# Kernel optimization log

Measured on AMD Instinct MI355X. Metric: run time of the kernel, lower is better.

The kernel has to match this reference:

```python
import jax, jax.numpy as jnp
import numpy as np

N = 100000      # nodes
E = 1600000     # directed edges (avg degree 16)
F_IN = 256      # dataset.num_node_features
HID = 64        # hidden
C = 40          # dataset.num_classes


def setup_inputs() -> dict:
    key = jax.random.key(0)
    k0, k1, k2, k3 = jax.random.split(key, 4)
    x = jax.random.normal(k0, (N, F_IN), dtype=jnp.float32)
    edge_index = jax.random.randint(k1, (2, E), 0, N, dtype=jnp.int32)
    # Glorot-style init like GCNConv.reset_parameters
    W1 = jax.random.normal(k2, (F_IN, HID), dtype=jnp.float32) * (1.0 / np.sqrt(F_IN))
    b1 = jnp.zeros((HID,), dtype=jnp.float32)
    W2 = jax.random.normal(k3, (HID, C), dtype=jnp.float32) * (1.0 / np.sqrt(HID))
    b2 = jnp.zeros((C,), dtype=jnp.float32)
    return {"x": x, "edge_index": edge_index, "W1": W1, "b1": b1, "W2": W2, "b2": b2}


def gcn_conv(x, row, col, norm, W, b):
    # PyG GCNConv: out[col] += norm * (x @ W)[row]; then + bias
    n = x.shape[0]
    h = x @ W                                   # [N, out]
    msg = h[row] * norm[:, None]                # [E+N, out] gather + scale
    out = jax.ops.segment_sum(msg, col, num_segments=n)  # scatter-add
    return out + b


def _norm_coeffs(edge_index, n, dtype):
    # add self-loops, then symmetric normalization D^{-1/2} A D^{-1/2}
    loop = jnp.arange(n, dtype=edge_index.dtype)
    row = jnp.concatenate([edge_index[0], loop])
    col = jnp.concatenate([edge_index[1], loop])
    deg = jax.ops.segment_sum(jnp.ones_like(col, dtype=dtype), col, num_segments=n)
    dis = jnp.where(deg > 0, jax.lax.rsqrt(jnp.maximum(deg, 1.0)), 0.0)
    return row, col, dis[row] * dis[col]


def reference(x, edge_index, W1, b1, W2, b2):
    n = x.shape[0]
    row, col, norm = _norm_coeffs(edge_index, n, x.dtype)
    h = jax.nn.relu(gcn_conv(x, row, col, norm, W1, b1))
    # F.dropout(p=0.5, training=False) is identity in eval mode
    out = gcn_conv(h, row, col, norm, W2, b2)
    return jax.nn.log_softmax(out, axis=1)
```

## Files before the change

### kernel.cpp

```cpp
#include <hip/hip_runtime.h>
#include <math.h>

#define N_NODES 100000
#define N_EDGES 1600000
#define F_INDIM 256
#define HID 64
#define NCLS 40
#define NBKT 196
#define NBLKA 196
#define EPB 8192
#define CAPB 96
#define REGSZ 12544
#define ECAP 10240
#define NGEMM1 391
#define KP 264
#define AP 72

typedef __attribute__((ext_vector_type(8))) short short8;
typedef __attribute__((ext_vector_type(4))) float floatx4;

__device__ __forceinline__ unsigned short f2bf(float f) {
  unsigned u = __float_as_uint(f);
  unsigned r = (u + 0x7FFFu + ((u >> 16) & 1u)) >> 16;
  return (unsigned short)r;
}
__device__ __forceinline__ void add8(float* a, uint4 u) {
  a[0] += __uint_as_float(u.x << 16);
  a[1] += __uint_as_float(u.x & 0xFFFF0000u);
  a[2] += __uint_as_float(u.y << 16);
  a[3] += __uint_as_float(u.y & 0xFFFF0000u);
  a[4] += __uint_as_float(u.z << 16);
  a[5] += __uint_as_float(u.z & 0xFFFF0000u);
  a[6] += __uint_as_float(u.w << 16);
  a[7] += __uint_as_float(u.w & 0xFFFF0000u);
}
__device__ __forceinline__ void fma8(float* a, float d, uint4 u) {
  a[0] = fmaf(d, __uint_as_float(u.x << 16), a[0]);
  a[1] = fmaf(d, __uint_as_float(u.x & 0xFFFF0000u), a[1]);
  a[2] = fmaf(d, __uint_as_float(u.y << 16), a[2]);
  a[3] = fmaf(d, __uint_as_float(u.y & 0xFFFF0000u), a[3]);
  a[4] = fmaf(d, __uint_as_float(u.z << 16), a[4]);
  a[5] = fmaf(d, __uint_as_float(u.z & 0xFFFF0000u), a[5]);
  a[6] = fmaf(d, __uint_as_float(u.w << 16), a[6]);
  a[7] = fmaf(d, __uint_as_float(u.w & 0xFFFF0000u), a[7]);
}


__global__ __launch_bounds__(1024) void k_pre(const int* __restrict__ row,
                                              const int* __restrict__ col,
                                              const float* __restrict__ x,
                                              const float* __restrict__ W1,
                                              unsigned int* __restrict__ bktdata,
                                              int* __restrict__ cnt,
                                              unsigned short* __restrict__ h1b) {
  __shared__ union {
    int cur[NBKT];
    unsigned short wt[HID * KP];
  } sm;
  const int t = threadIdx.x;

  if (blockIdx.x < NBLKA) {
    const int blk = blockIdx.x;
    const int e0 = blk * EPB;
    const int n = min(EPB, N_EDGES - e0);
    if (t < NBKT) sm.cur[t] = 0;
    __syncthreads();
    for (int i = t * 4; i < n; i += 4096) {
      int4 c4 = *(const int4*)&col[e0 + i];
      int4 r4 = *(const int4*)&row[e0 + i];
#pragma unroll
      for (int k = 0; k < 4; ++k) {
        int c = (k == 0) ? c4.x : (k == 1) ? c4.y : (k == 2) ? c4.z : c4.w;
        int r = (k == 0) ? r4.x : (k == 1) ? r4.y : (k == 2) ? r4.z : r4.w;
        int b = c >> 9;
        int p = atomicAdd(&sm.cur[b], 1);
        if (p < CAPB)
          bktdata[((size_t)b * NBLKA + blk) * CAPB + p] =
              ((unsigned)(c & 511) << 17) | (unsigned)r;
      }
    }
    __syncthreads();
    if (t < NBKT) cnt[t * NBLKA + blk] = min(sm.cur[t], CAPB);
  } else {
    const int lane = t & 63;
    const int w = t >> 6;
    const int quad = lane >> 4;
    const int l15 = lane & 15;
    const int rowBase = (blockIdx.x - NBLKA) * 256;
#pragma unroll
    for (int i = 0; i < 4; ++i) {
      int f = t + 1024 * i;
      int k = f >> 4;
      int n0 = (f & 15) * 4;
      float4 v = *(const float4*)&W1[(size_t)k * HID + n0];
      sm.wt[(n0 + 0) * KP + k] = f2bf(v.x);
      sm.wt[(n0 + 1) * KP + k] = f2bf(v.y);
      sm.wt[(n0 + 2) * KP + k] = f2bf(v.z);
      sm.wt[(n0 + 3) * KP + k] = f2bf(v.w);
    }
    __syncthreads();

    const int ar = rowBase + w * 16 + l15;
    const float* xrow =
        x + (size_t)((ar < N_NODES) ? ar : N_NODES - 1) * F_INDIM + quad * 8;

    floatx4 acc[4];
#pragma unroll
    for (int c = 0; c < 4; ++c) acc[c] = (floatx4){0.f, 0.f, 0.f, 0.f};

#pragma unroll
    for (int kc = 0; kc < F_INDIM; kc += 32) {
      const float4 va = *(const float4*)(xrow + kc);
      const float4 vb = *(const float4*)(xrow + kc + 4);
      short8 a;
      a[0] = (short)f2bf(va.x); a[1] = (short)f2bf(va.y);
      a[2] = (short)f2bf(va.z); a[3] = (short)f2bf(va.w);
      a[4] = (short)f2bf(vb.x); a[5] = (short)f2bf(vb.y);
      a[6] = (short)f2bf(vb.z); a[7] = (short)f2bf(vb.w);
#pragma unroll
      for (int c = 0; c < 4; ++c) {
        const short8 bfr = *(const short8*)&sm.wt[(c * 16 + l15) * KP + kc + quad * 8];
        acc[c] = __builtin_amdgcn_mfma_f32_16x16x32_bf16(a, bfr, acc[c], 0, 0, 0);
      }
    }

#pragma unroll
    for (int reg = 0; reg < 4; ++reg) {
      int gr = rowBase + w * 16 + quad * 4 + reg;
      if (gr <= N_NODES) {
        bool real = gr < N_NODES;
#pragma unroll
        for (int c = 0; c < 4; ++c)
          h1b[(size_t)gr * HID + c * 16 + l15] =
              real ? f2bf(acc[c][reg]) : (unsigned short)0;
      }
    }
  }
}


__global__ __launch_bounds__(1024) void k_build2(const int* __restrict__ cnt,
                                                 const unsigned int* __restrict__ bktdata,
                                                 float* __restrict__ dis,
                                                 int* __restrict__ start,
                                                 int* __restrict__ endi,
                                                 int* __restrict__ esrc) {
  __shared__ int scnt[NBLKA];
  __shared__ int sscan[NBLKA];
  __shared__ unsigned int ecache[ECAP];
  __shared__ int h[512];
  __shared__ int curs[512];
  __shared__ int sbase[512];
  const int b = blockIdx.x, t = threadIdx.x;

  if (t < 512) { h[t] = 0; curs[t] = 0; }
  if (t < NBLKA) { int c = cnt[b * NBLKA + t]; scnt[t] = c; sscan[t] = c; }
  __syncthreads();
#pragma unroll
  for (int off = 1; off < NBLKA; off <<= 1) {
    int u = (t < NBLKA && t >= off) ? sscan[t - off] : 0;
    __syncthreads();
    if (t < NBLKA) sscan[t] += u;
    __syncthreads();
  }
  const int total = min(sscan[NBLKA - 1], ECAP);

  for (int j = t; j < total; j += 1024) {
    int lo = 0, hi = NBLKA - 1;
    while (lo < hi) {
      int mid = (lo + hi) >> 1;
      if (sscan[mid] <= j) lo = mid + 1; else hi = mid;
    }
    int segoff = j - (sscan[lo] - scnt[lo]);
    ecache[j] = bktdata[((size_t)b * NBLKA + lo) * CAPB + segoff];
  }
  __syncthreads();

  for (int i = t; i < total; i += 1024) atomicAdd(&h[ecache[i] >> 17], 1);
  __syncthreads();

  int c0 = 0, p0 = 0;
  if (t < 512) {
    const int n0 = b * 512 + t;
    c0 = h[t];
    p0 = (c0 + 7) & ~7;
    if (n0 < N_NODES) dis[n0] = rsqrtf((float)(c0 + 1));
    else if (n0 == N_NODES) dis[n0] = 0.f;
    h[t] = p0;
  }
  __syncthreads();
#pragma unroll
  for (int off = 1; off < 512; off <<= 1) {
    int u = (t < 512 && t >= off) ? h[t - off] : 0;
    __syncthreads();
    if (t < 512) h[t] += u;
    __syncthreads();
  }
  if (t < 512) {
    const int n0 = b * 512 + t;
    const int sb0 = b * REGSZ + h[t] - p0;
    sbase[t] = sb0;
    if (n0 < N_NODES) { start[n0] = sb0; endi[n0] = sb0 + c0; }
    for (int k = c0; k < p0; ++k) esrc[sb0 + k] = N_NODES;
  }
  __syncthreads();

  for (int i = t; i < total; i += 1024) {
    unsigned u = ecache[i];
    int ld = u >> 17;
    int src = u & 0x1FFFF;
    int pos = sbase[ld] + atomicAdd(&curs[ld], 1);
    esrc[pos] = src;
  }
}


__global__ __launch_bounds__(512) void k_agg1g2(const int* __restrict__ esrc,
                                                const int* __restrict__ start,
                                                const int* __restrict__ endi,
                                                const float* __restrict__ dis,
                                                const unsigned short* __restrict__ h1b,
                                                const float* __restrict__ b1,
                                                const float* __restrict__ W2,
                                                unsigned short* __restrict__ gb) {
  __shared__ unsigned short as[64 * AP];
  __shared__ unsigned short w2t[48 * AP];
  const int t = threadIdx.x;
  const int nodeBase = blockIdx.x * 64;
  const int node = nodeBase + (t >> 3);
  const int q = t & 7;

  for (int i = t; i < 48 * 64; i += 512) {
    int nn = i >> 6;
    int k = i & 63;
    w2t[nn * AP + k] = (nn < NCLS) ? f2bf(W2[(size_t)k * NCLS + nn]) : (unsigned short)0;
  }

  uint4 o = (uint4){0u, 0u, 0u, 0u};
  if (node < N_NODES) {
    const uint4* hp4 = (const uint4*)h1b;
    const int s = start[node];
    const int e8 = (endi[node] + 7) & ~7;
    float acc[8];
#pragma unroll
    for (int j = 0; j < 8; ++j) acc[j] = 0.f;
    for (int i = s; i < e8; i += 8) {
      int4 sa = *(const int4*)&esrc[i];
      int4 sb = *(const int4*)&esrc[i + 4];
      float d0 = dis[sa.x], d1 = dis[sa.y], d2 = dis[sa.z], d3 = dis[sa.w];
      float d4 = dis[sb.x], d5 = dis[sb.y], d6 = dis[sb.z], d7 = dis[sb.w];
      uint4 u0 = hp4[(size_t)sa.x * 8 + q];
      uint4 u1 = hp4[(size_t)sa.y * 8 + q];
      uint4 u2 = hp4[(size_t)sa.z * 8 + q];
      uint4 u3 = hp4[(size_t)sa.w * 8 + q];
      uint4 u4 = hp4[(size_t)sb.x * 8 + q];
      uint4 u5 = hp4[(size_t)sb.y * 8 + q];
      uint4 u6 = hp4[(size_t)sb.z * 8 + q];
      uint4 u7 = hp4[(size_t)sb.w * 8 + q];
      fma8(acc, d0, u0); fma8(acc, d1, u1); fma8(acc, d2, u2); fma8(acc, d3, u3);
      fma8(acc, d4, u4); fma8(acc, d5, u5); fma8(acc, d6, u6); fma8(acc, d7, u7);
    }
    const float dn = dis[node];
    uint4 us = hp4[(size_t)node * 8 + q];
    fma8(acc, dn, us);
    float4 ba = *(const float4*)&b1[q * 8];
    float4 bb = *(const float4*)&b1[q * 8 + 4];
    float v0 = fmaxf(dn * acc[0] + ba.x, 0.f);
    float v1 = fmaxf(dn * acc[1] + ba.y, 0.f);
    float v2 = fmaxf(dn * acc[2] + ba.z, 0.f);
    float v3 = fmaxf(dn * acc[3] + ba.w, 0.f);
    float v4 = fmaxf(dn * acc[4] + bb.x, 0.f);
    float v5 = fmaxf(dn * acc[5] + bb.y, 0.f);
    float v6 = fmaxf(dn * acc[6] + bb.z, 0.f);
    float v7 = fmaxf(dn * acc[7] + bb.w, 0.f);
    o.x = (unsigned)f2bf(v0) | ((unsigned)f2bf(v1) << 16);
    o.y = (unsigned)f2bf(v2) | ((unsigned)f2bf(v3) << 16);
    o.z = (unsigned)f2bf(v4) | ((unsigned)f2bf(v5) << 16);
    o.w = (unsigned)f2bf(v6) | ((unsigned)f2bf(v7) << 16);
  }
  *(uint4*)&as[(t >> 3) * AP + q * 8] = o;
  __syncthreads();

  const int lane = t & 63;
  const int w = t >> 6;
  if (w < 4) {
    const int quad = lane >> 4;
    const int l15 = lane & 15;
    floatx4 acc2[3];
#pragma unroll
    for (int c = 0; c < 3; ++c) acc2[c] = (floatx4){0.f, 0.f, 0.f, 0.f};
#pragma unroll
    for (int kh = 0; kh < 2; ++kh) {
      const short8 a = *(const short8*)&as[(w * 16 + l15) * AP + kh * 32 + quad * 8];
#pragma unroll
      for (int c = 0; c < 3; ++c) {
        const short8 bfr = *(const short8*)&w2t[(c * 16 + l15) * AP + kh * 32 + quad * 8];
        acc2[c] = __builtin_amdgcn_mfma_f32_16x16x32_bf16(a, bfr, acc2[c], 0, 0, 0);
      }
    }
#pragma unroll
    for (int reg = 0; reg < 4; ++reg) {
      int gr = nodeBase + w * 16 + quad * 4 + reg;
      if (gr <= N_NODES) {
        float dd = dis[gr];
#pragma unroll
        for (int c = 0; c < 3; ++c)
          gb[(size_t)gr * 64 + c * 16 + l15] = f2bf(dd * acc2[c][reg]);
        gb[(size_t)gr * 64 + 48 + l15] = 0;
      }
    }
  }
}


__global__ __launch_bounds__(256) void k_agg2ls(const int* __restrict__ esrc,
                                                const int* __restrict__ start,
                                                const int* __restrict__ endi,
                                                const float* __restrict__ dis,
                                                const unsigned short* __restrict__ gb,
                                                const float* __restrict__ b2,
                                                float* __restrict__ out) {
  int gid = blockIdx.x * 256 + threadIdx.x;
  int node = gid >> 3;
  int q = gid & 7;
  if (node >= N_NODES) return;
  const uint4* gp4 = (const uint4*)gb;
  const int s = start[node];
  const int e8 = (endi[node] + 7) & ~7;
  float acc[8];
#pragma unroll
  for (int j = 0; j < 8; ++j) acc[j] = 0.f;
  for (int i = s; i < e8; i += 8) {
    int4 sa = *(const int4*)&esrc[i];
    int4 sb = *(const int4*)&esrc[i + 4];
    uint4 u0 = gp4[(size_t)sa.x * 8 + q];
    uint4 u1 = gp4[(size_t)sa.y * 8 + q];
    uint4 u2 = gp4[(size_t)sa.z * 8 + q];
    uint4 u3 = gp4[(size_t)sa.w * 8 + q];
    uint4 u4 = gp4[(size_t)sb.x * 8 + q];
    uint4 u5 = gp4[(size_t)sb.y * 8 + q];
    uint4 u6 = gp4[(size_t)sb.z * 8 + q];
    uint4 u7 = gp4[(size_t)sb.w * 8 + q];
    add8(acc, u0); add8(acc, u1); add8(acc, u2); add8(acc, u3);
    add8(acc, u4); add8(acc, u5); add8(acc, u6); add8(acc, u7);
  }
  uint4 us = gp4[(size_t)node * 8 + q];
  add8(acc, us);
  const bool wr = q < 5;
  float v0 = 0.f, v1 = 0.f, v2 = 0.f, v3 = 0.f, v4 = 0.f, v5 = 0.f, v6 = 0.f, v7 = 0.f;
  float m = -INFINITY;
  if (wr) {
    float d = dis[node];
    float4 ba = *(const float4*)&b2[q * 8];
    float4 bb = *(const float4*)&b2[q * 8 + 4];
    v0 = d * acc[0] + ba.x;
    v1 = d * acc[1] + ba.y;
    v2 = d * acc[2] + ba.z;
    v3 = d * acc[3] + ba.w;
    v4 = d * acc[4] + bb.x;
    v5 = d * acc[5] + bb.y;
    v6 = d * acc[6] + bb.z;
    v7 = d * acc[7] + bb.w;
    m = fmaxf(fmaxf(fmaxf(v0, v1), fmaxf(v2, v3)),
              fmaxf(fmaxf(v4, v5), fmaxf(v6, v7)));
  }
#pragma unroll
  for (int off = 1; off < 8; off <<= 1) m = fmaxf(m, __shfl_xor(m, off));
  float el = 0.f;
  if (wr) {
    el = __expf(v0 - m) + __expf(v1 - m) + __expf(v2 - m) + __expf(v3 - m) +
         __expf(v4 - m) + __expf(v5 - m) + __expf(v6 - m) + __expf(v7 - m);
  }
#pragma unroll
  for (int off = 1; off < 8; off <<= 1) el += __shfl_xor(el, off);
  float ls = logf(el);
  if (wr) {
    float4 o1 = make_float4(v0 - m - ls, v1 - m - ls, v2 - m - ls, v3 - m - ls);
    float4 o2 = make_float4(v4 - m - ls, v5 - m - ls, v6 - m - ls, v7 - m - ls);
    *(float4*)&out[(size_t)node * NCLS + q * 8] = o1;
    *(float4*)&out[(size_t)node * NCLS + q * 8 + 4] = o2;
  }
}


extern "C" void kernel_launch(void* const* d_in, const int* in_sizes, int n_in,
                              void* d_out, int out_size, void* d_ws, size_t ws_size,
                              hipStream_t stream) {
  const float* x  = (const float*)d_in[0];
  const int*   ei = (const int*)d_in[1];
  const float* W1 = (const float*)d_in[2];
  const float* b1 = (const float*)d_in[3];
  const float* W2 = (const float*)d_in[4];
  const float* b2 = (const float*)d_in[5];
  float* out = (float*)d_out;

  const int* row = ei;
  const int* col = ei + N_EDGES;

  int*            esrc    = (int*)d_ws;
  unsigned int*   bktdata = (unsigned int*)(esrc + (size_t)NBKT * REGSZ);
  int*            cnt     = (int*)(bktdata + (size_t)NBKT * NBLKA * CAPB);
  unsigned short* h1b     = (unsigned short*)(cnt + NBKT * NBLKA);
  unsigned short* gb      = h1b + (size_t)(N_NODES + 1) * HID;
  float*          dis     = (float*)(gb + (size_t)(N_NODES + 1) * HID);
  int*            start   = (int*)(dis + N_NODES + 1);
  int*            endi    = start + N_NODES + 1;

  k_pre<<<NBLKA + NGEMM1, 1024, 0, stream>>>(row, col, x, W1, bktdata, cnt, h1b);
  k_build2<<<NBKT, 1024, 0, stream>>>(cnt, bktdata, dis, start, endi, esrc);
  k_agg1g2<<<(N_NODES + 63) / 64, 512, 0, stream>>>(esrc, start, endi, dis, h1b, b1, W2, gb);
  k_agg2ls<<<(N_NODES * 8 + 255) / 256, 256, 0, stream>>>(esrc, start, endi, dis, gb, b2, out);
}
```

Baseline: 316.2 us.

## Prescale layer-1 features by dis and split aggregation from second GEMM

```diff
diff --git a/kernel.cpp b/kernel.cpp
--- a/kernel.cpp
+++ b/kernel.cpp
@@ -34,16 +34,6 @@
   a[6] += __uint_as_float(u.w << 16);
   a[7] += __uint_as_float(u.w & 0xFFFF0000u);
 }
-__device__ __forceinline__ void fma8(float* a, float d, uint4 u) {
-  a[0] = fmaf(d, __uint_as_float(u.x << 16), a[0]);
-  a[1] = fmaf(d, __uint_as_float(u.x & 0xFFFF0000u), a[1]);
-  a[2] = fmaf(d, __uint_as_float(u.y << 16), a[2]);
-  a[3] = fmaf(d, __uint_as_float(u.y & 0xFFFF0000u), a[3]);
-  a[4] = fmaf(d, __uint_as_float(u.z << 16), a[4]);
-  a[5] = fmaf(d, __uint_as_float(u.z & 0xFFFF0000u), a[5]);
-  a[6] = fmaf(d, __uint_as_float(u.w << 16), a[6]);
-  a[7] = fmaf(d, __uint_as_float(u.w & 0xFFFF0000u), a[7]);
-}
 
 
 __global__ __launch_bounds__(1024) void k_pre(const int* __restrict__ row,
@@ -144,13 +134,15 @@
                                                  float* __restrict__ dis,
                                                  int* __restrict__ start,
                                                  int* __restrict__ endi,
-                                                 int* __restrict__ esrc) {
+                                                 int* __restrict__ esrc,
+                                                 unsigned short* __restrict__ h1b) {
   __shared__ int scnt[NBLKA];
   __shared__ int sscan[NBLKA];
   __shared__ unsigned int ecache[ECAP];
   __shared__ int h[512];
   __shared__ int curs[512];
   __shared__ int sbase[512];
+  __shared__ float sdis[512];
   const int b = blockIdx.x, t = threadIdx.x;
 
   if (t < 512) { h[t] = 0; curs[t] = 0; }
@@ -184,8 +176,9 @@
     const int n0 = b * 512 + t;
     c0 = h[t];
     p0 = (c0 + 7) & ~7;
-    if (n0 < N_NODES) dis[n0] = rsqrtf((float)(c0 + 1));
-    else if (n0 == N_NODES) dis[n0] = 0.f;
+    float dv = rsqrtf((float)(c0 + 1));
+    sdis[t] = (n0 < N_NODES) ? dv : 0.f;
+    if (n0 < N_NODES) dis[n0] = dv;
     h[t] = p0;
   }
   __syncthreads();
@@ -212,102 +205,137 @@
     int pos = sbase[ld] + atomicAdd(&curs[ld], 1);
     esrc[pos] = src;
   }
-}
-
-
-__global__ __launch_bounds__(512) void k_agg1g2(const int* __restrict__ esrc,
-                                                const int* __restrict__ start,
-                                                const int* __restrict__ endi,
-                                                const float* __restrict__ dis,
-                                                const unsigned short* __restrict__ h1b,
-                                                const float* __restrict__ b1,
-                                                const float* __restrict__ W2,
-                                                unsigned short* __restrict__ gb) {
+
+  uint4* h4 = (uint4*)h1b;
+  for (int i = t; i < 512 * 8; i += 1024) {
+    int r = i >> 3, qq = i & 7;
+    int n0 = b * 512 + r;
+    if (n0 < N_NODES) {
+      float d = sdis[r];
+      uint4 u = h4[(size_t)n0 * 8 + qq];
+      float f0 = __uint_as_float(u.x << 16) * d;
+      float f1 = __uint_as_float(u.x & 0xFFFF0000u) * d;
+      float f2 = __uint_as_float(u.y << 16) * d;
+      float f3 = __uint_as_float(u.y & 0xFFFF0000u) * d;
+      float f4 = __uint_as_float(u.z << 16) * d;
+      float f5 = __uint_as_float(u.z & 0xFFFF0000u) * d;
+      float f6 = __uint_as_float(u.w << 16) * d;
+      float f7 = __uint_as_float(u.w & 0xFFFF0000u) * d;
+      u.x = (unsigned)f2bf(f0) | ((unsigned)f2bf(f1) << 16);
+      u.y = (unsigned)f2bf(f2) | ((unsigned)f2bf(f3) << 16);
+      u.z = (unsigned)f2bf(f4) | ((unsigned)f2bf(f5) << 16);
+      u.w = (unsigned)f2bf(f6) | ((unsigned)f2bf(f7) << 16);
+      h4[(size_t)n0 * 8 + qq] = u;
+    }
+  }
+}
+
+
+__global__ __launch_bounds__(256) void k_agg1(const int* __restrict__ esrc,
+                                              const int* __restrict__ start,
+                                              const int* __restrict__ endi,
+                                              const float* __restrict__ dis,
+                                              const unsigned short* __restrict__ h1b,
+                                              const float* __restrict__ b1,
+                                              unsigned short* __restrict__ ab) {
+  int gid = blockIdx.x * 256 + threadIdx.x;
+  int node = gid >> 3;
+  int q = gid & 7;
+  if (node >= N_NODES) return;
+  const uint4* hp4 = (const uint4*)h1b;
+  const int s = start[node];
+  const int e8 = (endi[node] + 7) & ~7;
+  float acc[8];
+#pragma unroll
+  for (int j = 0; j < 8; ++j) acc[j] = 0.f;
+  for (int i = s; i < e8; i += 8) {
+    int4 sa = *(const int4*)&esrc[i];
+    int4 sb = *(const int4*)&esrc[i + 4];
+    uint4 u0 = hp4[(size_t)sa.x * 8 + q];
+    uint4 u1 = hp4[(size_t)sa.y * 8 + q];
+    uint4 u2 = hp4[(size_t)sa.z * 8 + q];
+    uint4 u3 = hp4[(size_t)sa.w * 8 + q];
+    uint4 u4 = hp4[(size_t)sb.x * 8 + q];
+    uint4 u5 = hp4[(size_t)sb.y * 8 + q];
+    uint4 u6 = hp4[(size_t)sb.z * 8 + q];
+    uint4 u7 = hp4[(size_t)sb.w * 8 + q];
+    add8(acc, u0); add8(acc, u1); add8(acc, u2); add8(acc, u3);
+    add8(acc, u4); add8(acc, u5); add8(acc, u6); add8(acc, u7);
+  }
+  uint4 us = hp4[(size_t)node * 8 + q];
+  add8(acc, us);
+  float d = dis[node];
+  float4 ba = *(const float4*)&b1[q * 8];
+  float4 bb = *(const float4*)&b1[q * 8 + 4];
+  float v0 = fmaxf(d * acc[0] + ba.x, 0.f);
+  float v1 = fmaxf(d * acc[1] + ba.y, 0.f);
+  float v2 = fmaxf(d * acc[2] + ba.z, 0.f);
+  float v3 = fmaxf(d * acc[3] + ba.w, 0.f);
+  float v4 = fmaxf(d * acc[4] + bb.x, 0.f);
+  float v5 = fmaxf(d * acc[5] + bb.y, 0.f);
+  float v6 = fmaxf(d * acc[6] + bb.z, 0.f);
+  float v7 = fmaxf(d * acc[7] + bb.w, 0.f);
+  uint4 o;
+  o.x = (unsigned)f2bf(v0) | ((unsigned)f2bf(v1) << 16);
+  o.y = (unsigned)f2bf(v2) | ((unsigned)f2bf(v3) << 16);
+  o.z = (unsigned)f2bf(v4) | ((unsigned)f2bf(v5) << 16);
+  o.w = (unsigned)f2bf(v6) | ((unsigned)f2bf(v7) << 16);
+  ((uint4*)ab)[(size_t)node * 8 + q] = o;
+}
+
+
+__global__ __launch_bounds__(256) void k_gemm2(const unsigned short* __restrict__ ab,
+                                               const float* __restrict__ W2,
+                                               const float* __restrict__ dis,
+                                               unsigned short* __restrict__ gb) {
   __shared__ unsigned short as[64 * AP];
   __shared__ unsigned short w2t[48 * AP];
-  const int t = threadIdx.x;
-  const int nodeBase = blockIdx.x * 64;
-  const int node = nodeBase + (t >> 3);
-  const int q = t & 7;
-
-  for (int i = t; i < 48 * 64; i += 512) {
-    int nn = i >> 6;
+  const int tid = threadIdx.x;
+  const int lane = tid & 63;
+  const int w = tid >> 6;
+  const int quad = lane >> 4;
+  const int l15 = lane & 15;
+  const int rowBase = blockIdx.x * 64;
+
+  for (int i = tid; i < 48 * 64; i += 256) {
+    int n = i >> 6;
     int k = i & 63;
-    w2t[nn * AP + k] = (nn < NCLS) ? f2bf(W2[(size_t)k * NCLS + nn]) : (unsigned short)0;
-  }
-
-  uint4 o = (uint4){0u, 0u, 0u, 0u};
-  if (node < N_NODES) {
-    const uint4* hp4 = (const uint4*)h1b;
-    const int s = start[node];
-    const int e8 = (endi[node] + 7) & ~7;
-    float acc[8];
-#pragma unroll
-    for (int j = 0; j < 8; ++j) acc[j] = 0.f;
-    for (int i = s; i < e8; i += 8) {
-      int4 sa = *(const int4*)&esrc[i];
-      int4 sb = *(const int4*)&esrc[i + 4];
-      float d0 = dis[sa.x], d1 = dis[sa.y], d2 = dis[sa.z], d3 = dis[sa.w];
-      float d4 = dis[sb.x], d5 = dis[sb.y], d6 = dis[sb.z], d7 = dis[sb.w];
-      uint4 u0 = hp4[(size_t)sa.x * 8 + q];
-      uint4 u1 = hp4[(size_t)sa.y * 8 + q];
-      uint4 u2 = hp4[(size_t)sa.z * 8 + q];
-      uint4 u3 = hp4[(size_t)sa.w * 8 + q];
-      uint4 u4 = hp4[(size_t)sb.x * 8 + q];
-      uint4 u5 = hp4[(size_t)sb.y * 8 + q];
-      uint4 u6 = hp4[(size_t)sb.z * 8 + q];
-      uint4 u7 = hp4[(size_t)sb.w * 8 + q];
-      fma8(acc, d0, u0); fma8(acc, d1, u1); fma8(acc, d2, u2); fma8(acc, d3, u3);
-      fma8(acc, d4, u4); fma8(acc, d5, u5); fma8(acc, d6, u6); fma8(acc, d7, u7);
-    }
-    const float dn = dis[node];
-    uint4 us = hp4[(size_t)node * 8 + q];
-    fma8(acc, dn, us);
-    float4 ba = *(const float4*)&b1[q * 8];
-    float4 bb = *(const float4*)&b1[q * 8 + 4];
-    float v0 = fmaxf(dn * acc[0] + ba.x, 0.f);
-    float v1 = fmaxf(dn * acc[1] + ba.y, 0.f);
-    float v2 = fmaxf(dn * acc[2] + ba.z, 0.f);
-    float v3 = fmaxf(dn * acc[3] + ba.w, 0.f);
-    float v4 = fmaxf(dn * acc[4] + bb.x, 0.f);
-    float v5 = fmaxf(dn * acc[5] + bb.y, 0.f);
-    float v6 = fmaxf(dn * acc[6] + bb.z, 0.f);
-    float v7 = fmaxf(dn * acc[7] + bb.w, 0.f);
-    o.x = (unsigned)f2bf(v0) | ((unsigned)f2bf(v1) << 16);
-    o.y = (unsigned)f2bf(v2) | ((unsigned)f2bf(v3) << 16);
-    o.z = (unsigned)f2bf(v4) | ((unsigned)f2bf(v5) << 16);
-    o.w = (unsigned)f2bf(v6) | ((unsigned)f2bf(v7) << 16);
-  }
-  *(uint4*)&as[(t >> 3) * AP + q * 8] = o;
-  __syncthreads();
-
-  const int lane = t & 63;
-  const int w = t >> 6;
-  if (w < 4) {
-    const int quad = lane >> 4;
-    const int l15 = lane & 15;
-    floatx4 acc2[3];
-#pragma unroll
-    for (int c = 0; c < 3; ++c) acc2[c] = (floatx4){0.f, 0.f, 0.f, 0.f};
-#pragma unroll
-    for (int kh = 0; kh < 2; ++kh) {
-      const short8 a = *(const short8*)&as[(w * 16 + l15) * AP + kh * 32 + quad * 8];
-#pragma unroll
-      for (int c = 0; c < 3; ++c) {
-        const short8 bfr = *(const short8*)&w2t[(c * 16 + l15) * AP + kh * 32 + quad * 8];
-        acc2[c] = __builtin_amdgcn_mfma_f32_16x16x32_bf16(a, bfr, acc2[c], 0, 0, 0);
-      }
-    }
-#pragma unroll
-    for (int reg = 0; reg < 4; ++reg) {
-      int gr = nodeBase + w * 16 + quad * 4 + reg;
-      if (gr <= N_NODES) {
-        float dd = dis[gr];
-#pragma unroll
-        for (int c = 0; c < 3; ++c)
-          gb[(size_t)gr * 64 + c * 16 + l15] = f2bf(dd * acc2[c][reg]);
-        gb[(size_t)gr * 64 + 48 + l15] = 0;
-      }
+    w2t[n * AP + k] = (n < NCLS) ? f2bf(W2[(size_t)k * NCLS + n]) : (unsigned short)0;
+  }
+#pragma unroll
+  for (int i = 0; i < 2; ++i) {
+    int f = tid + 256 * i;
+    int r = f >> 3;
+    int q = f & 7;
+    int gr = rowBase + r;
+    short8 v = (short8){0, 0, 0, 0, 0, 0, 0, 0};
+    if (gr < N_NODES) v = *(const short8*)&ab[(size_t)gr * HID + q * 8];
+    *(short8*)&as[r * AP + q * 8] = v;
+  }
+  __syncthreads();
+
+  floatx4 acc[3];
+#pragma unroll
+  for (int c = 0; c < 3; ++c) acc[c] = (floatx4){0.f, 0.f, 0.f, 0.f};
+
+#pragma unroll
+  for (int kh = 0; kh < 2; ++kh) {
+    const short8 a = *(const short8*)&as[(w * 16 + l15) * AP + kh * 32 + quad * 8];
+#pragma unroll
+    for (int c = 0; c < 3; ++c) {
+      const short8 bfr = *(const short8*)&w2t[(c * 16 + l15) * AP + kh * 32 + quad * 8];
+      acc[c] = __builtin_amdgcn_mfma_f32_16x16x32_bf16(a, bfr, acc[c], 0, 0, 0);
+    }
+  }
+
+#pragma unroll
+  for (int reg = 0; reg < 4; ++reg) {
+    int gr = rowBase + w * 16 + quad * 4 + reg;
+    if (gr < N_NODES) {
+      float d = dis[gr];
+#pragma unroll
+      for (int c = 0; c < 3; ++c)
+        gb[(size_t)gr * 64 + c * 16 + l15] = f2bf(d * acc[c][reg]);
     }
   }
 }
@@ -324,29 +352,31 @@
   int node = gid >> 3;
   int q = gid & 7;
   if (node >= N_NODES) return;
-  const uint4* gp4 = (const uint4*)gb;
-  const int s = start[node];
-  const int e8 = (endi[node] + 7) & ~7;
+  const bool wr = q < 5;
   float acc[8];
 #pragma unroll
   for (int j = 0; j < 8; ++j) acc[j] = 0.f;
-  for (int i = s; i < e8; i += 8) {
-    int4 sa = *(const int4*)&esrc[i];
-    int4 sb = *(const int4*)&esrc[i + 4];
-    uint4 u0 = gp4[(size_t)sa.x * 8 + q];
-    uint4 u1 = gp4[(size_t)sa.y * 8 + q];
-    uint4 u2 = gp4[(size_t)sa.z * 8 + q];
-    uint4 u3 = gp4[(size_t)sa.w * 8 + q];
-    uint4 u4 = gp4[(size_t)sb.x * 8 + q];
-    uint4 u5 = gp4[(size_t)sb.y * 8 + q];
-    uint4 u6 = gp4[(size_t)sb.z * 8 + q];
-    uint4 u7 = gp4[(size_t)sb.w * 8 + q];
-    add8(acc, u0); add8(acc, u1); add8(acc, u2); add8(acc, u3);
-    add8(acc, u4); add8(acc, u5); add8(acc, u6); add8(acc, u7);
-  }
-  uint4 us = gp4[(size_t)node * 8 + q];
-  add8(acc, us);
-  const bool wr = q < 5;
+  if (wr) {
+    const uint4* gp4 = (const uint4*)gb;
+    const int s = start[node];
+    const int e8 = (endi[node] + 7) & ~7;
+    for (int i = s; i < e8; i += 8) {
+      int4 sa = *(const int4*)&esrc[i];
+      int4 sb = *(const int4*)&esrc[i + 4];
+      uint4 u0 = gp4[(size_t)sa.x * 8 + q];
+      uint4 u1 = gp4[(size_t)sa.y * 8 + q];
+      uint4 u2 = gp4[(size_t)sa.z * 8 + q];
+      uint4 u3 = gp4[(size_t)sa.w * 8 + q];
+      uint4 u4 = gp4[(size_t)sb.x * 8 + q];
+      uint4 u5 = gp4[(size_t)sb.y * 8 + q];
+      uint4 u6 = gp4[(size_t)sb.z * 8 + q];
+      uint4 u7 = gp4[(size_t)sb.w * 8 + q];
+      add8(acc, u0); add8(acc, u1); add8(acc, u2); add8(acc, u3);
+      add8(acc, u4); add8(acc, u5); add8(acc, u6); add8(acc, u7);
+    }
+    uint4 us = gp4[(size_t)node * 8 + q];
+    add8(acc, us);
+  }
   float v0 = 0.f, v1 = 0.f, v2 = 0.f, v3 = 0.f, v4 = 0.f, v5 = 0.f, v6 = 0.f, v7 = 0.f;
   float m = -INFINITY;
   if (wr) {
@@ -401,13 +431,15 @@
   unsigned int*   bktdata = (unsigned int*)(esrc + (size_t)NBKT * REGSZ);
   int*            cnt     = (int*)(bktdata + (size_t)NBKT * NBLKA * CAPB);
   unsigned short* h1b     = (unsigned short*)(cnt + NBKT * NBLKA);
-  unsigned short* gb      = h1b + (size_t)(N_NODES + 1) * HID;
-  float*          dis     = (float*)(gb + (size_t)(N_NODES + 1) * HID);
-  int*            start   = (int*)(dis + N_NODES + 1);
-  int*            endi    = start + N_NODES + 1;
+  unsigned short* ab      = h1b + (size_t)(N_NODES + 1) * HID;
+  float*          dis     = (float*)(ab + (size_t)N_NODES * HID);
+  int*            start   = (int*)(dis + N_NODES);
+  int*            endi    = start + N_NODES;
+  unsigned short* gb      = h1b;
 
   k_pre<<<NBLKA + NGEMM1, 1024, 0, stream>>>(row, col, x, W1, bktdata, cnt, h1b);
-  k_build2<<<NBKT, 1024, 0, stream>>>(cnt, bktdata, dis, start, endi, esrc);
-  k_agg1g2<<<(N_NODES + 63) / 64, 512, 0, stream>>>(esrc, start, endi, dis, h1b, b1, W2, gb);
+  k_build2<<<NBKT, 1024, 0, stream>>>(cnt, bktdata, dis, start, endi, esrc, h1b);
+  k_agg1<<<(N_NODES * 8 + 255) / 256, 256, 0, stream>>>(esrc, start, endi, dis, h1b, b1, ab);
+  k_gemm2<<<(N_NODES + 63) / 64, 256, 0, stream>>>(ab, W2, dis, gb);
   k_agg2ls<<<(N_NODES * 8 + 255) / 256, 256, 0, stream>>>(esrc, start, endi, dis, gb, b2, out);
 }
```

New measurement: 322.9 us. 2.1% more time.
